# Kernel tuning notes

Measured on AMD Instinct MI355X. Metric: run time of the kernel, lower is better.

Reference implementation:

```python
import jax, jax.numpy as jnp
import numpy as np

EPS = 1e-12  # torch f.normalize eps


def _rms_norm(x, g):
    # f.normalize(x, dim=1) * g * sqrt(C): L2-normalize over channel dim
    c = x.shape[1]
    n = jnp.maximum(jnp.linalg.norm(x, axis=1, keepdims=True), EPS)
    return x / n * g * (c ** 0.5)


def setup_inputs() -> dict:
    key = jax.random.key(0)
    ks = jax.random.split(key, 5)
    b, dim, H, W = 32, 256, 64, 64
    heads, dim_head, num_mem = 4, 32, 4
    hidden = heads * dim_head
    return {
        "x": jax.random.normal(ks[0], (b, dim, H, W), dtype=jnp.float32),
        "g1": jnp.ones((1, dim, 1, 1), dtype=jnp.float32),
        "mem_kv": jax.random.normal(ks[1], (2, heads, dim_head, num_mem), dtype=jnp.float32),
        "w_qkv": jax.random.normal(ks[2], (3 * hidden, dim), dtype=jnp.float32) * (1.0 / np.sqrt(dim)),
        "w_out": jax.random.normal(ks[3], (dim, hidden), dtype=jnp.float32) * (1.0 / np.sqrt(hidden)),
        "b_out": jnp.zeros((dim,), dtype=jnp.float32),
        "g2": jnp.ones((1, dim, 1, 1), dtype=jnp.float32),
    }


def reference(x, g1, mem_kv, w_qkv, w_out, b_out, g2):
    b, c, H, W = x.shape
    _, heads, dim_head, num_mem = mem_kv.shape
    n = H * W
    scale = dim_head ** -0.5

    xn = _rms_norm(x, g1)
    # 1x1 conv qkv projection: [b, 3*hidden, H, W]
    qkv = jnp.einsum('oc,bchw->bohw', w_qkv, xn)
    hidden = heads * dim_head
    q, k, v = jnp.split(qkv, 3, axis=1)
    # b (h d) x y -> b h d (x y)
    q = q.reshape(b, heads, dim_head, n)
    k = k.reshape(b, heads, dim_head, n)
    v = v.reshape(b, heads, dim_head, n)

    mk = jnp.broadcast_to(mem_kv[0], (b, heads, dim_head, num_mem))
    mv = jnp.broadcast_to(mem_kv[1], (b, heads, dim_head, num_mem))
    k = jnp.concatenate([mk, k], axis=-1)
    v = jnp.concatenate([mv, v], axis=-1)

    q = jax.nn.softmax(q, axis=-2) * scale  # softmax over head dim d
    k = jax.nn.softmax(k, axis=-1)          # softmax over sequence n

    context = jnp.einsum('bhdn,bhen->bhde', k, v)   # [b,h,d,e]
    out = jnp.einsum('bhde,bhdn->bhen', context, q)  # [b,h,e,n]
    out = out.reshape(b, hidden, H, W)

    o = jnp.einsum('oc,bchw->bohw', w_out, out) + b_out[None, :, None, None]
    return _rms_norm(o, g2)
```

## Files before the change

### kernel.cpp

```cpp
#include <hip/hip_runtime.h>
#include <math.h>

#define CC   256
#define HW   4096
#define OC3  384
#define HID  128
#define DH   32
#define NM   4
#define NPART 8
#define SCALE 0.17677669529663688f

typedef __bf16 bf16x8 __attribute__((ext_vector_type(8)));
typedef float  f32x4  __attribute__((ext_vector_type(4)));

__device__ __forceinline__ ushort f2bf(float x) {
    union { float f; unsigned u; } v; v.f = x;
    unsigned r = v.u + 0x7fffu + ((v.u >> 16) & 1u);
    return (ushort)(r >> 16);
}
__device__ __forceinline__ float bf2f(ushort b) {
    union { unsigned u; float f; } v; v.u = ((unsigned)b) << 16; return v.f;
}
__device__ __forceinline__ void g2l16(const void* g, void* l) {
    __builtin_amdgcn_global_load_lds(
        (const __attribute__((address_space(1))) void*)g,
        (__attribute__((address_space(3))) void*)l, 16, 0, 0);
}

__global__ void k_prep(const float* __restrict__ wqkv, const float* __restrict__ g1,
                       const float* __restrict__ wout,
                       ushort* __restrict__ wq2t, ushort* __restrict__ woutt) {
    int o = blockIdx.x, t = threadIdx.x;
    wq2t[(size_t)o * CC + t] = f2bf(wqkv[(size_t)o * CC + t] * g1[t] * 16.0f);
    if (o < CC && t < HID) woutt[(size_t)o * HID + t] = f2bf(wout[(size_t)o * HID + t]);
}

__global__ __launch_bounds__(256) void k_qkv(const ushort* __restrict__ wq2t,
        const float* __restrict__ x, ushort* __restrict__ qkv) {
    __shared__ __align__(16) ushort As[2][128 * 32];
    __shared__ __align__(16) ushort Bs[2][128 * 40];
    __shared__ float nrm[256];
    __shared__ float invp[128];
    int tid = threadIdx.x;
    int lin = blockIdx.x + 3 * (blockIdx.y + 32 * blockIdx.z);
    int swz = (lin & 7) * 384 + (lin >> 3);
    int m0 = (swz % 3) * 128;
    int t_ = swz / 3;
    int p0 = (t_ & 31) * 128;
    int b  = t_ >> 5;
    int lane = tid & 63, wid = tid >> 6;
    int l15 = tid & 15, quad = (tid >> 4) & 3;
    int wm = wid >> 1, wn = wid & 1;
    int rsub = lane >> 2, csub = (lane & 3) * 8;
    int tpix = tid & 127;
    int tc8  = (tid >> 7) * 8;
    const ushort* Ab = wq2t + (size_t)m0 * CC;
    const float*  xg = x + ((size_t)b * CC) * HW + p0 + tpix;
    float psum = 0.f;
    f32x4 acc[4][4];
    #pragma unroll
    for (int i = 0; i < 4; ++i)
        #pragma unroll
        for (int j = 0; j < 4; ++j) acc[i][j] = (f32x4){0.f, 0.f, 0.f, 0.f};

    auto stage = [&](int buf, int k0) {
        float xv[16];
        #pragma unroll
        for (int i = 0; i < 8; ++i) xv[i]     = xg[(size_t)(k0 + tc8 + i) * HW];
        #pragma unroll
        for (int i = 0; i < 8; ++i) xv[8 + i] = xg[(size_t)(k0 + tc8 + 16 + i) * HW];
        uint4 pka, pkb; ushort* oa = (ushort*)&pka; ushort* ob = (ushort*)&pkb;
        #pragma unroll
        for (int i = 0; i < 8; ++i) { float v = xv[i];     psum += v * v; oa[i] = f2bf(v); }
        #pragma unroll
        for (int i = 0; i < 8; ++i) { float v = xv[8 + i]; psum += v * v; ob[i] = f2bf(v); }
        *(uint4*)&Bs[buf][tpix * 40 + tc8]      = pka;
        *(uint4*)&Bs[buf][tpix * 40 + tc8 + 16] = pkb;
        #pragma unroll
        for (int q = 0; q < 2; ++q) {
            int rw = wid * 32 + q * 16;
            g2l16(Ab + (size_t)(rw + rsub) * CC + k0 + csub, &As[buf][rw * 32]);
        }
    };

    stage(0, 0);
    __syncthreads();
    #pragma unroll
    for (int s = 0; s < 8; ++s) {
        int cur = s & 1;
        bf16x8 af[4], bfr[4];
        #pragma unroll
        for (int mt = 0; mt < 4; ++mt)
            af[mt] = *(const bf16x8*)&As[cur][(wm * 64 + mt * 16 + l15) * 32 + quad * 8];
        #pragma unroll
        for (int nt = 0; nt < 4; ++nt)
            bfr[nt] = *(const bf16x8*)&Bs[cur][(wn * 64 + nt * 16 + l15) * 40 + quad * 8];
        #pragma unroll
        for (int mt = 0; mt < 4; ++mt)
            #pragma unroll
            for (int nt = 0; nt < 4; ++nt)
                acc[mt][nt] = __builtin_amdgcn_mfma_f32_16x16x32_bf16(
                                  af[mt], bfr[nt], acc[mt][nt], 0, 0, 0);
        if (s < 7) stage(cur ^ 1, (s + 1) * 32);
        __syncthreads();
    }
    nrm[tid] = psum;
    __syncthreads();
    if (tid < 128) {
        float s = nrm[tid] + nrm[tid + 128];
        invp[tid] = 1.0f / fmaxf(sqrtf(s), 1e-12f);
    }
    __syncthreads();
    #pragma unroll
    for (int mt = 0; mt < 4; ++mt) {
        int o = m0 + wm * 64 + mt * 16 + quad * 4;
        #pragma unroll
        for (int nt = 0; nt < 4; ++nt) {
            int pixl = wn * 64 + nt * 16 + l15;
            float iv = invp[pixl];
            ushort* dst = qkv + ((size_t)(b * OC3 + o)) * HW + p0 + pixl;
            #pragma unroll
            for (int r = 0; r < 4; ++r) dst[(size_t)r * HW] = f2bf(acc[mt][nt][r] * iv);
        }
    }
}

__global__ void k_ksoft(const ushort* __restrict__ qkv, const float* __restrict__ memkv,
                        float* __restrict__ kmaxb, float* __restrict__ rsumb) {
    int row = blockIdx.x * 4 + (threadIdx.x >> 6);
    int lane = threadIdx.x & 63;
    int b = row >> 7, hd = row & 127;
    const ushort* kp = qkv + ((size_t)(b * OC3 + HID + hd)) * HW;
    float m = -1e30f;
    #pragma unroll
    for (int i0 = 0; i0 < HW; i0 += 512) {
        uint4 pk = *(const uint4*)&kp[i0 + lane * 8];
        const ushort* e = (const ushort*)&pk;
        #pragma unroll
        for (int j = 0; j < 8; ++j) m = fmaxf(m, bf2f(e[j]));
    }
    #pragma unroll
    for (int s = 1; s < 64; s <<= 1) m = fmaxf(m, __shfl_xor(m, s));
    const float* mk = memkv + hd * NM;
    #pragma unroll
    for (int j = 0; j < NM; ++j) m = fmaxf(m, mk[j]);
    float s = 0.f;
    #pragma unroll
    for (int i0 = 0; i0 < HW; i0 += 512) {
        uint4 pk = *(const uint4*)&kp[i0 + lane * 8];
        const ushort* e = (const ushort*)&pk;
        #pragma unroll
        for (int j = 0; j < 8; ++j) s += __expf(bf2f(e[j]) - m);
    }
    #pragma unroll
    for (int t = 1; t < 64; t <<= 1) s += __shfl_xor(s, t);
    #pragma unroll
    for (int j = 0; j < NM; ++j) s += __expf(mk[j] - m);
    if (lane == 0) { kmaxb[row] = m; rsumb[row] = 1.0f / s; }
}

__global__ __launch_bounds__(256) void k_ctx(const ushort* __restrict__ qkv,
        const float* __restrict__ memkv, const float* __restrict__ kmaxb,
        const float* __restrict__ rsumb, float* __restrict__ ctxp) {
    __shared__ float kl[DH][65];
    __shared__ float vl[DH][65];
    __shared__ float red[256 * 33];
    int tid = threadIdx.x;
    int bh = blockIdx.x;
    int part = blockIdx.y;
    int b = bh >> 2, h = bh & 3;
    int lr = tid >> 3;
    int nn8 = (tid & 7) * 8;
    const ushort* kp = qkv + ((size_t)(b * OC3 + HID + h * DH) + lr) * HW + part * 512 + nn8;
    const ushort* vp = qkv + ((size_t)(b * OC3 + 2 * HID + h * DH) + lr) * HW + part * 512 + nn8;
    int rowbase = bh * DH;
    float kmr = kmaxb[rowbase + lr], rsr = rsumb[rowbase + lr];
    int slot = tid & 31, nng = tid >> 5;
    int d0 = (slot >> 2) * 4, e0 = (slot & 3) * 8;
    float acc[4][8];
    #pragma unroll
    for (int i = 0; i < 4; ++i)
        #pragma unroll
        for (int j = 0; j < 8; ++j) acc[i][j] = 0.f;
    for (int n0 = 0; n0 < 512; n0 += 64) {
        __syncthreads();
        uint4 kv4 = *(const uint4*)&kp[n0];
        uint4 vv4 = *(const uint4*)&vp[n0];
        const ushort* ke = (const ushort*)&kv4;
        const ushort* ve = (const ushort*)&vv4;
        #pragma unroll
        for (int j = 0; j < 8; ++j) {
            kl[lr][nn8 + j] = __expf(bf2f(ke[j]) - kmr) * rsr;
            vl[lr][nn8 + j] = bf2f(ve[j]);
        }
        __syncthreads();
        #pragma unroll 2
        for (int t = 0; t < 8; ++t) {
            int nn = nng * 8 + t;
            float kv[4], vv[8];
            #pragma unroll
            for (int i = 0; i < 4; ++i) kv[i] = kl[d0 + i][nn];
            #pragma unroll
            for (int j = 0; j < 8; ++j) vv[j] = vl[e0 + j][nn];
            #pragma unroll
            for (int i = 0; i < 4; ++i)
                #pragma unroll
                for (int j = 0; j < 8; ++j) acc[i][j] += kv[i] * vv[j];
        }
    }
    __syncthreads();
    #pragma unroll
    for (int i = 0; i < 4; ++i)
        #pragma unroll
        for (int j = 0; j < 8; ++j) red[tid * 33 + i * 8 + j] = acc[i][j];
    __syncthreads();
    #pragma unroll
    for (int q = 0; q < 4; ++q) {
        int o = tid * 4 + q;
        int d = o >> 5, e = o & 31;
        int sl = (d >> 2) * 4 + (e >> 3);
        int k = (d & 3) * 8 + (e & 7);
        float s = 0.f;
        #pragma unroll
        for (int g = 0; g < 8; ++g) s += red[(g * 32 + sl) * 33 + k];
        if (part == 0) {
            float km = kmaxb[rowbase + d], rsm = rsumb[rowbase + d];
            #pragma unroll
            for (int m = 0; m < NM; ++m) {
                float kw = __expf(memkv[(h * DH + d) * NM + m] - km) * rsm;
                s += kw * memkv[512 + (h * DH + e) * NM + m];
            }
        }
        ctxp[(size_t)part * 131072 + (size_t)bh * 1024 + o] = s;
    }
}

__global__ __launch_bounds__(256) void k_w2(const float* __restrict__ ctxp,
        const ushort* __restrict__ woutt, ushort* __restrict__ W2) {
    __shared__ ushort ctxb[4 * 32 * 40];
    int tid = threadIdx.x, b = blockIdx.x;
    int wid = tid >> 6;
    int l15 = tid & 15, quad = (tid >> 4) & 3;
    #pragma unroll
    for (int j = 0; j < 16; ++j) {
        int idx = tid + j * 256;
        float s = 0.f;
        #pragma unroll
        for (int p = 0; p < NPART; ++p)
            s += ctxp[(size_t)p * 131072 + (size_t)b * 4096 + idx];
        int h = idx >> 10, d = (idx >> 5) & 31, e = idx & 31;
        ctxb[(h * 32 + d) * 40 + e] = f2bf(s);
    }
    __syncthreads();
    #pragma unroll
    for (int h = 0; h < 4; ++h) {
        f32x4 acc[4][2];
        #pragma unroll
        for (int i = 0; i < 4; ++i)
            #pragma unroll
            for (int j = 0; j < 2; ++j) acc[i][j] = (f32x4){0.f, 0.f, 0.f, 0.f};
        bf16x8 af[4], bfr[2];
        #pragma unroll
        for (int mt = 0; mt < 4; ++mt)
            af[mt] = *(const bf16x8*)&woutt[(size_t)(wid * 64 + mt * 16 + l15) * HID
                                            + h * DH + quad * 8];
        #pragma unroll
        for (int nt = 0; nt < 2; ++nt)
            bfr[nt] = *(const bf16x8*)&ctxb[(h * 32 + nt * 16 + l15) * 40 + quad * 8];
        #pragma unroll
        for (int mt = 0; mt < 4; ++mt)
            #pragma unroll
            for (int nt = 0; nt < 2; ++nt)
                acc[mt][nt] = __builtin_amdgcn_mfma_f32_16x16x32_bf16(
                                  af[mt], bfr[nt], acc[mt][nt], 0, 0, 0);
        #pragma unroll
        for (int mt = 0; mt < 4; ++mt)
            #pragma unroll
            for (int nt = 0; nt < 2; ++nt)
                #pragma unroll
                for (int r = 0; r < 4; ++r) {
                    int oc = wid * 64 + mt * 16 + quad * 4 + r;
                    int d  = nt * 16 + l15;
                    W2[((size_t)b * CC + oc) * HID + h * DH + d] = f2bf(acc[mt][nt][r]);
                }
    }
}

__global__ __launch_bounds__(256) void k_final(const ushort* __restrict__ qkv,
        const ushort* __restrict__ W2, const float* __restrict__ bout,
        const float* __restrict__ g2, float* __restrict__ y) {
    __shared__ __align__(16) ushort sq[64 * 136];
    __shared__ __align__(16) ushort Ws[256 * 32];
    __shared__ float red[64 * 17];
    __shared__ float invs[64];
    __shared__ float bl[256];
    __shared__ float gl[256];
    int tid = threadIdx.x;
    int b = blockIdx.y;
    int hwb = blockIdx.x * 64;
    int lane = tid & 63, wid = tid >> 6;
    int l15 = tid & 15, quad = (tid >> 4) & 3;
    bl[tid] = bout[tid];
    gl[tid] = g2[tid];

    {
        const ushort* qp = qkv + ((size_t)b * OC3 + wid * DH) * HW + hwb + lane;
        float vd[32];
        float m = -1e30f;
        #pragma unroll
        for (int d = 0; d < 32; ++d) {
            float v = bf2f(qp[(size_t)d * HW]);
            vd[d] = v; m = fmaxf(m, v);
        }
        float s = 0.f;
        #pragma unroll
        for (int d = 0; d < 32; ++d) { float e = __expf(vd[d] - m); vd[d] = e; s += e; }
        float r_ = SCALE / s;
        #pragma unroll
        for (int q8 = 0; q8 < 4; ++q8) {
            uint4 pk; ushort* o8 = (ushort*)&pk;
            #pragma unroll
            for (int i = 0; i < 8; ++i) o8[i] = f2bf(vd[q8 * 8 + i] * r_);
            *(uint4*)&sq[lane * 136 + wid * DH + q8 * 8] = pk;
        }
    }

    f32x4 acc[4][4];
    #pragma unroll
    for (int i = 0; i < 4; ++i)
        #pragma unroll
        for (int j = 0; j < 4; ++j) acc[i][j] = (f32x4){0.f, 0.f, 0.f, 0.f};
    int rsub = lane >> 2, csub = (lane & 3) * 8;
    const ushort* W2b = W2 + (size_t)b * CC * HID;
    for (int k0 = 0; k0 < HID; k0 += 32) {
        __syncthreads();
        #pragma unroll
        for (int q = 0; q < 4; ++q) {
            int rw = wid * 64 + q * 16;
            g2l16(W2b + (size_t)(rw + rsub) * HID + k0 + csub, &Ws[rw * 32]);
        }
        __syncthreads();
        bf16x8 af[4], bfr[4];
        #pragma unroll
        for (int mt = 0; mt < 4; ++mt)
            af[mt] = *(const bf16x8*)&Ws[(wid * 64 + mt * 16 + l15) * 32 + quad * 8];
        #pragma unroll
        for (int nt = 0; nt < 4; ++nt)
            bfr[nt] = *(const bf16x8*)&sq[(nt * 16 + l15) * 136 + k0 + quad * 8];
        #pragma unroll
        for (int mt = 0; mt < 4; ++mt)
            #pragma unroll
            for (int nt = 0; nt < 4; ++nt)
                acc[mt][nt] = __builtin_amdgcn_mfma_f32_16x16x32_bf16(
                                  af[mt], bfr[nt], acc[mt][nt], 0, 0, 0);
    }

    float part[4] = {0.f, 0.f, 0.f, 0.f};
    #pragma unroll
    for (int mt = 0; mt < 4; ++mt)
        #pragma unroll
        for (int r = 0; r < 4; ++r) {
            int oc = wid * 64 + mt * 16 + quad * 4 + r;
            float bo = bl[oc];
            #pragma unroll
            for (int nt = 0; nt < 4; ++nt) {
                float v = acc[mt][nt][r] + bo;
                acc[mt][nt][r] = v;
                part[nt] += v * v;
            }
        }
    __syncthreads();
    #pragma unroll
    for (int nt = 0; nt < 4; ++nt)
        red[(nt * 16 + l15) * 17 + wid * 4 + quad] = part[nt];
    __syncthreads();
    if (tid < 64) {
        float s = 0.f;
        #pragma unroll
        for (int g = 0; g < 16; ++g) s += red[tid * 17 + g];
        invs[tid] = 1.0f / fmaxf(sqrtf(s), 1e-12f);
    }
    __syncthreads();
    #pragma unroll
    for (int mt = 0; mt < 4; ++mt)
        #pragma unroll
        for (int nt = 0; nt < 4; ++nt) {
            int pix = nt * 16 + l15;
            float iv = invs[pix];
            #pragma unroll
            for (int r = 0; r < 4; ++r) {
                int oc = wid * 64 + mt * 16 + quad * 4 + r;
                y[((size_t)(b * CC + oc)) * HW + hwb + pix] = acc[mt][nt][r] * iv * gl[oc] * 16.0f;
            }
        }
}

extern "C" void kernel_launch(void* const* d_in, const int* in_sizes, int n_in,
                              void* d_out, int out_size, void* d_ws, size_t ws_size,
                              hipStream_t stream) {
    const float* x     = (const float*)d_in[0];
    const float* g1    = (const float*)d_in[1];
    const float* memkv = (const float*)d_in[2];
    const float* wqkv  = (const float*)d_in[3];
    const float* wout  = (const float*)d_in[4];
    const float* bout  = (const float*)d_in[5];
    const float* g2    = (const float*)d_in[6];
    float* y = (float*)d_out;

    char* w = (char*)d_ws;
    ushort* wq2t  = (ushort*)w;  w += (size_t)OC3 * CC * 2;
    ushort* woutt = (ushort*)w;  w += (size_t)CC * HID * 2;
    float*  kmaxb = (float*)w;   w += 4096 * 4;
    float*  rsumb = (float*)w;   w += 4096 * 4;
    float*  ctxp  = (float*)w;   w += (size_t)NPART * 131072 * 4;
    ushort* W2    = (ushort*)w;  w += (size_t)32 * CC * HID * 2;
    ushort* qkv   = (ushort*)w;  w += (size_t)32 * OC3 * HW * 2;

    k_prep  <<<dim3(384),       dim3(256), 0, stream>>>(wqkv, g1, wout, wq2t, woutt);
    k_qkv   <<<dim3(3, 32, 32), dim3(256), 0, stream>>>(wq2t, x, qkv);
    k_ksoft <<<dim3(1024),      dim3(256), 0, stream>>>(qkv, memkv, kmaxb, rsumb);
    k_ctx   <<<dim3(128, 8),    dim3(256), 0, stream>>>(qkv, memkv, kmaxb, rsumb, ctxp);
    k_w2    <<<dim3(32),        dim3(256), 0, stream>>>(ctxp, woutt, W2);
    k_final <<<dim3(64, 32),    dim3(256), 0, stream>>>(qkv, W2, bout, g2, y);
}
```

Measured before the change: 422.4 us.

## Prefetch x loads before MFMA and XOR-swizzle LDS tiles in qkv GEMM

The staging of the next K-slice is split in the qkv projection kernel. Global loads of x are now issued into registers before the current MFMA block, and the bf16 conversion and LDS write happen only after it, so load latency overlaps compute. The padded LDS B layout (stride 40) is replaced by an unpadded stride-32 layout with an XOR swizzle, and the same swizzle is applied to the A tile loaded via global_load_lds. This removes bank conflicts without padding, at the cost of extra live registers for the prefetched x values.

```diff
diff --git a/kernel.cpp b/kernel.cpp
--- a/kernel.cpp
+++ b/kernel.cpp
@@ -38,7 +38,7 @@
 __global__ __launch_bounds__(256) void k_qkv(const ushort* __restrict__ wq2t,
         const float* __restrict__ x, ushort* __restrict__ qkv) {
     __shared__ __align__(16) ushort As[2][128 * 32];
-    __shared__ __align__(16) ushort Bs[2][128 * 40];
+    __shared__ __align__(16) ushort Bs[2][128 * 32];
     __shared__ float nrm[256];
     __shared__ float invp[128];
     int tid = threadIdx.x;
@@ -51,59 +51,78 @@
     int lane = tid & 63, wid = tid >> 6;
     int l15 = tid & 15, quad = (tid >> 4) & 3;
     int wm = wid >> 1, wn = wid & 1;
-    int rsub = lane >> 2, csub = (lane & 3) * 8;
+    int rsub = lane >> 2;
     int tpix = tid & 127;
-    int tc8  = (tid >> 7) * 8;
+    int grp  = tid >> 7;
+    int bsw  = (tpix >> 1) & 3;
     const ushort* Ab = wq2t + (size_t)m0 * CC;
     const float*  xg = x + ((size_t)b * CC) * HW + p0 + tpix;
     float psum = 0.f;
+    float xv[16];
     f32x4 acc[4][4];
     #pragma unroll
     for (int i = 0; i < 4; ++i)
         #pragma unroll
         for (int j = 0; j < 4; ++j) acc[i][j] = (f32x4){0.f, 0.f, 0.f, 0.f};
 
-    auto stage = [&](int buf, int k0) {
-        float xv[16];
-        #pragma unroll
-        for (int i = 0; i < 8; ++i) xv[i]     = xg[(size_t)(k0 + tc8 + i) * HW];
-        #pragma unroll
-        for (int i = 0; i < 8; ++i) xv[8 + i] = xg[(size_t)(k0 + tc8 + 16 + i) * HW];
+    auto issueB = [&](int k0) {
+        #pragma unroll
+        for (int i = 0; i < 8; ++i) xv[i]     = xg[(size_t)(k0 + grp * 8 + i) * HW];
+        #pragma unroll
+        for (int i = 0; i < 8; ++i) xv[8 + i] = xg[(size_t)(k0 + grp * 8 + 16 + i) * HW];
+    };
+    auto writeB = [&](int buf) {
         uint4 pka, pkb; ushort* oa = (ushort*)&pka; ushort* ob = (ushort*)&pkb;
         #pragma unroll
         for (int i = 0; i < 8; ++i) { float v = xv[i];     psum += v * v; oa[i] = f2bf(v); }
         #pragma unroll
         for (int i = 0; i < 8; ++i) { float v = xv[8 + i]; psum += v * v; ob[i] = f2bf(v); }
-        *(uint4*)&Bs[buf][tpix * 40 + tc8]      = pka;
-        *(uint4*)&Bs[buf][tpix * 40 + tc8 + 16] = pkb;
+        *(uint4*)&Bs[buf][tpix * 32 + (( grp      ^ bsw) << 3)] = pka;
+        *(uint4*)&Bs[buf][tpix * 32 + (((grp + 2) ^ bsw) << 3)] = pkb;
+    };
+    auto stageA = [&](int buf, int k0) {
         #pragma unroll
         for (int q = 0; q < 2; ++q) {
             int rw = wid * 32 + q * 16;
-            g2l16(Ab + (size_t)(rw + rsub) * CC + k0 + csub, &As[buf][rw * 32]);
+            int r  = rw + rsub;
+            int slog = (lane & 3) ^ ((r >> 1) & 3);
+            g2l16(Ab + (size_t)r * CC + k0 + slog * 8, &As[buf][rw * 32]);
         }
     };
 
-    stage(0, 0);
-    __syncthreads();
+    issueB(0);
+    stageA(0, 0);
+    writeB(0);
+    __syncthreads();
+
     #pragma unroll
     for (int s = 0; s < 8; ++s) {
         int cur = s & 1;
+        if (s < 7) {
+            issueB((s + 1) * 32);
+            stageA(cur ^ 1, (s + 1) * 32);
+        }
         bf16x8 af[4], bfr[4];
         #pragma unroll
-        for (int mt = 0; mt < 4; ++mt)
-            af[mt] = *(const bf16x8*)&As[cur][(wm * 64 + mt * 16 + l15) * 32 + quad * 8];
-        #pragma unroll
-        for (int nt = 0; nt < 4; ++nt)
-            bfr[nt] = *(const bf16x8*)&Bs[cur][(wn * 64 + nt * 16 + l15) * 40 + quad * 8];
+        for (int mt = 0; mt < 4; ++mt) {
+            int ra = wm * 64 + mt * 16 + l15;
+            af[mt] = *(const bf16x8*)&As[cur][ra * 32 + ((quad ^ ((ra >> 1) & 3)) << 3)];
+        }
+        #pragma unroll
+        for (int nt = 0; nt < 4; ++nt) {
+            int rb = wn * 64 + nt * 16 + l15;
+            bfr[nt] = *(const bf16x8*)&Bs[cur][rb * 32 + ((quad ^ ((rb >> 1) & 3)) << 3)];
+        }
         #pragma unroll
         for (int mt = 0; mt < 4; ++mt)
             #pragma unroll
             for (int nt = 0; nt < 4; ++nt)
                 acc[mt][nt] = __builtin_amdgcn_mfma_f32_16x16x32_bf16(
                                   af[mt], bfr[nt], acc[mt][nt], 0, 0, 0);
-        if (s < 7) stage(cur ^ 1, (s + 1) * 32);
+        if (s < 7) writeB(cur ^ 1);
         __syncthreads();
     }
+
     nrm[tid] = psum;
     __syncthreads();
     if (tid < 128) {
```

Result: faster. 376.4 us (-10.9%).
